# Optimization experiments

Measured on AMD Instinct MI355X. Metric: run time of the kernel, lower is better.

The kernel has to match this reference:

```python
import jax, jax.numpy as jnp
import numpy as np

# Module hyperparameters (from init_kwargs)
KH, KW = 3, 3
STRIDE_H = STRIDE_W = 1
PAD_H = PAD_W = 1
DIL_H = DIL_W = 1
DEFORM_GROUPS = 1
IN_CH, OUT_CH = 64, 64


def setup_inputs() -> dict:
    key = jax.random.key(0)
    k1, k2, k3, k4 = jax.random.split(key, 4)
    B, C, H, W = 4, IN_CH, 128, 128
    K = KH * KW
    x = jax.random.normal(k1, (B, C, H, W), dtype=jnp.float32)
    offset = jax.random.normal(k2, (B, DEFORM_GROUPS * 2 * K, H, W), dtype=jnp.float32)
    mask = jax.random.uniform(k3, (B, DEFORM_GROUPS * K, H, W), dtype=jnp.float32)
    stdv = 1.0 / np.sqrt(C * KH * KW)
    weight = jax.random.uniform(k4, (OUT_CH, C, KH, KW), dtype=jnp.float32,
                                minval=-stdv, maxval=stdv)
    bias = jnp.zeros((OUT_CH,), dtype=jnp.float32)
    return {"x": x, "offset": offset, "mask": mask, "weight": weight, "bias": bias}


def _bilinear_gather(img, ys, xs):
    """img: [N,Cg,H,W]; ys,xs: [N,K,Ho,Wo] absolute pixel coords.
    Returns [N,K,Ho,Wo,Cg]; zero padding outside, matches torch grid_sample
    (align_corners=False, padding_mode='zeros')."""
    N, Cg, H, W = img.shape
    y0f = jnp.floor(ys)
    x0f = jnp.floor(xs)
    wy = (ys - y0f)[..., None]
    wx = (xs - x0f)[..., None]
    y0 = y0f.astype(jnp.int32)
    x0 = x0f.astype(jnp.int32)
    b = jnp.arange(N)[:, None, None, None]

    def g(yi, xi):
        valid = (yi >= 0) & (yi < H) & (xi >= 0) & (xi < W)
        v = img[b, :, jnp.clip(yi, 0, H - 1), jnp.clip(xi, 0, W - 1)]  # [N,K,Ho,Wo,Cg]
        return jnp.where(valid[..., None], v, jnp.zeros((), img.dtype))

    v00 = g(y0, x0)
    v01 = g(y0, x0 + 1)
    v10 = g(y0 + 1, x0)
    v11 = g(y0 + 1, x0 + 1)
    return (v00 * (1 - wy) * (1 - wx) + v01 * (1 - wy) * wx
            + v10 * wy * (1 - wx) + v11 * wy * wx)


def _mdcn(x, offset, mask, weight, bias):
    B, C, H, W = x.shape
    O = weight.shape[0]
    K = KH * KW
    G = DEFORM_GROUPS
    Cg = C // G
    Ho = (H + 2 * PAD_H - (DIL_H * (KH - 1) + 1)) // STRIDE_H + 1
    Wo = (W + 2 * PAD_W - (DIL_W * (KW - 1) + 1)) // STRIDE_W + 1

    base_y = jnp.arange(Ho, dtype=x.dtype) * STRIDE_H - PAD_H          # [Ho]
    base_x = jnp.arange(Wo, dtype=x.dtype) * STRIDE_W - PAD_W          # [Wo]
    ky = (jnp.arange(K) // KW).astype(x.dtype) * DIL_H                 # [K]
    kx = (jnp.arange(K) % KW).astype(x.dtype) * DIL_W                  # [K]

    off = offset.reshape(B, G, K, 2, Ho, Wo)
    sy = (base_y[None, None, None, :, None] + ky[None, None, :, None, None]
          + off[:, :, :, 0])                                           # [B,G,K,Ho,Wo]
    sx = (base_x[None, None, None, None, :] + kx[None, None, :, None, None]
          + off[:, :, :, 1])

    img = x.reshape(B * G, Cg, H, W)
    sampled = _bilinear_gather(img, sy.reshape(B * G, K, Ho, Wo),
                               sx.reshape(B * G, K, Ho, Wo))            # [B*G,K,Ho,Wo,Cg]
    sampled = sampled * mask.reshape(B * G, K, Ho, Wo)[..., None]
    sampled = sampled.reshape(B, G, K, Ho, Wo, Cg)

    w = weight.reshape(O, G, Cg, K)
    out = jnp.einsum('bgkhwc,ogck->bohw', sampled, w)
    return out + bias[None, :, None, None]


def reference(x, offset, mask, weight, bias):
    return _mdcn(x, offset, mask, weight, bias)
```

## Files before the change

### kernel.cpp

```cpp
#include <hip/hip_runtime.h>
#include <hip/hip_bf16.h>
#include <math.h>

constexpr int B = 4, C = 64, H = 128, W = 128, K = 9, O = 64;
constexpr int HXW = H * W;

typedef _Float16 half8 __attribute__((ext_vector_type(8)));
typedef float f32x4 __attribute__((ext_vector_type(4)));

__global__ void wt_kernel(const float* __restrict__ weight, float* __restrict__ wt) {
    int idx = blockIdx.x * 256 + threadIdx.x;
    if (idx >= K * C * O) return;
    int o = idx & 63;
    int c = (idx >> 6) & 63;
    int k = idx >> 12;
    wt[idx] = weight[(o * C + c) * K + k];
}

__global__ __launch_bounds__(256) void mdcn_nchw(
        const float* __restrict__ x, const float* __restrict__ offset,
        const float* __restrict__ mask, const float* __restrict__ wt,
        const float* __restrict__ bias, float* __restrict__ out) {
    int pid = blockIdx.x * 256 + threadIdx.x;
    int b = pid >> 14;
    int hw = pid & (HXW - 1);
    int h = hw >> 7;
    int w = hw & 127;
    float acc[O];
#pragma unroll
    for (int o = 0; o < O; ++o) acc[o] = bias[o];
#pragma unroll 1
    for (int k = 0; k < K; ++k) {
        float offy = offset[((size_t)(b * 2 * K + 2 * k)) * HXW + hw];
        float offx = offset[((size_t)(b * 2 * K + 2 * k + 1)) * HXW + hw];
        float m    = mask[((size_t)(b * K + k)) * HXW + hw];
        float sy = (float)(h - 1 + k / 3) + offy;
        float sx = (float)(w - 1 + k % 3) + offx;
        float y0f = floorf(sy), x0f = floorf(sx);
        float wy = sy - y0f, wx = sx - x0f;
        int y0 = (int)y0f, x0 = (int)x0f;
        int y1 = y0 + 1, x1 = x0 + 1;
        bool vy0 = (y0 >= 0) & (y0 < H), vy1 = (y1 >= 0) & (y1 < H);
        bool vx0 = (x0 >= 0) & (x0 < W), vx1 = (x1 >= 0) & (x1 < W);
        float w00 = (vy0 & vx0) ? (1.0f - wy) * (1.0f - wx) * m : 0.0f;
        float w01 = (vy0 & vx1) ? (1.0f - wy) * wx * m : 0.0f;
        float w10 = (vy1 & vx0) ? wy * (1.0f - wx) * m : 0.0f;
        float w11 = (vy1 & vx1) ? wy * wx * m : 0.0f;
        int y0c = min(max(y0, 0), H - 1), y1c = min(max(y1, 0), H - 1);
        int x0c = min(max(x0, 0), W - 1), x1c = min(max(x1, 0), W - 1);
        const float* p00 = x + (size_t)b * C * HXW + y0c * W + x0c;
        const float* p01 = x + (size_t)b * C * HXW + y0c * W + x1c;
        const float* p10 = x + (size_t)b * C * HXW + y1c * W + x0c;
        const float* p11 = x + (size_t)b * C * HXW + y1c * W + x1c;
        const float* wk = wt + k * C * O;
#pragma unroll 1
        for (int c0 = 0; c0 < C; c0 += 4) {
            float v[4];
#pragma unroll
            for (int j = 0; j < 4; ++j) {
                size_t cs = (size_t)(c0 + j) * HXW;
                v[j] = w00 * p00[cs] + w01 * p01[cs] + w10 * p10[cs] + w11 * p11[cs];
            }
            const float* wr = wk + c0 * O;
#pragma unroll
            for (int j = 0; j < 4; ++j)
#pragma unroll
                for (int o = 0; o < O; ++o) acc[o] = fmaf(wr[j * O + o], v[j], acc[o]);
        }
    }
#pragma unroll
    for (int o = 0; o < O; ++o) out[((size_t)(b * O + o)) * HXW + hw] = acc[o];
}

constexpr int XT_BLOCKS = B * HXW / 128;
__global__ __launch_bounds__(256) void prep_kernel(
        const float* __restrict__ x, const float* __restrict__ weight,
        _Float16* __restrict__ xht, _Float16* __restrict__ wth) {
    int bid = blockIdx.x;
    if (bid < XT_BLOCKS) {
        __shared__ float lds[128 * 65];
        int t = threadIdx.x;
        int P = bid * 128;
        int b = P >> 14;
        int hw0 = P & (HXW - 1);
        int px = t & 127;
        int hf = t >> 7;
        const float* src = x + (size_t)b * C * HXW + hw0 + px;
#pragma unroll
        for (int cc = 0; cc < 32; ++cc) {
            int ch = hf * 32 + cc;
            lds[px * 65 + ch] = src[(size_t)ch * HXW];
        }
        __syncthreads();
        _Float16* dst = xht + ((size_t)b * HXW + hw0 + px) * 64 + hf * 32;
        const float* row = lds + px * 65 + hf * 32;
#pragma unroll
        for (int j = 0; j < 4; ++j) {
            half8 pk;
#pragma unroll
            for (int e = 0; e < 8; ++e) pk[e] = (_Float16)row[j * 8 + e];
            *(half8*)(dst + j * 8) = pk;
        }
    } else {
        int idx = (bid - XT_BLOCKS) * 256 + threadIdx.x;
        if (idx < K * O * C) {
            int e = idx & 7;
            int lane = (idx >> 3) & 63;
            int s = (idx >> 9) & 7;
            int k = idx >> 12;
            int ml = lane & 15, kg = lane >> 4;
            int nf = s & 3, ks = s >> 2;
            int o = nf * 16 + ml;
            int c = ks * 32 + kg * 8 + e;
            wth[idx] = (_Float16)weight[(o * C + c) * K + k];
        }
    }
}

__global__ __launch_bounds__(1024, 1) void mdcn_f16(
        const _Float16* __restrict__ xht,
        const float* __restrict__ offset,
        const float* __restrict__ mask,
        const _Float16* __restrict__ wth,
        const float* __restrict__ bias,
        float* __restrict__ out) {
    __shared__ _Float16 Wlds[K * 8 * 64 * 8];
    __shared__ _Float16 Alds[16][16 * 64];

    int bid = blockIdx.x;
    int slab = bid & 7;
    int within = bid >> 3;
    int tid = threadIdx.x;
    int lane = tid & 63;
    int wid = tid >> 6;
    int ml = lane & 15, kg = lane >> 4;
    int p8 = lane >> 3, ch8 = lane & 7;
    int b = slab >> 1;
    int hwblk = (slab & 1) * 8192 + within * 256;
    int h = (hwblk >> 7) + (wid >> 3);
    int wbase = (wid & 7) * 16;
    int hwwave = h * 128 + wbase;
    _Float16* Aw = &Alds[wid][0];

#pragma unroll
    for (int j = 0; j < 5; ++j) {
        int idx = tid + j * 1024;
        if (idx < K * 8 * 64) *(half8*)(Wlds + idx * 8) = *(const half8*)(wth + idx * 8);
    }
    __syncthreads();

    f32x4 acc[4];
#pragma unroll
    for (int nf = 0; nf < 4; ++nf) {
        float bv = bias[nf * 16 + ml];
        acc[nf] = (f32x4){bv, bv, bv, bv};
    }

    const _Float16* xb = xht + (size_t)b * HXW * 64;
    const float* offb = offset + (size_t)b * 2 * K * HXW;
    const float* mskb = mask + (size_t)b * K * HXW;

    float oy[2], ox[2], mm[2];
#pragma unroll
    for (int g = 0; g < 2; ++g) {
        int hw = hwwave + g * 8 + p8;
        oy[g] = offb[hw];
        ox[g] = offb[(size_t)HXW + hw];
        mm[g] = mskb[hw];
    }

#pragma unroll 1
    for (int k = 0; k < K; ++k) {
        int ky = k / 3 - 1, kx = k % 3 - 1;

        float w00[2], w01[2], w10[2], w11[2];
        int r00[2], r01[2], r10[2], r11[2];
#pragma unroll
        for (int g = 0; g < 2; ++g) {
            int pl = g * 8 + p8;
            int w = wbase + pl;
            float sy = (float)(h + ky) + oy[g];
            float sx = (float)(w + kx) + ox[g];
            float y0f = floorf(sy), x0f = floorf(sx);
            float wy = sy - y0f, wx = sx - x0f;
            int y0 = (int)y0f, x0 = (int)x0f;
            int y1 = y0 + 1, x1 = x0 + 1;
            bool vy0 = (y0 >= 0) & (y0 < H), vy1 = (y1 >= 0) & (y1 < H);
            bool vx0 = (x0 >= 0) & (x0 < W), vx1 = (x1 >= 0) & (x1 < W);
            float m = mm[g];
            w00[g] = (vy0 & vx0) ? (1.0f - wy) * (1.0f - wx) * m : 0.0f;
            w01[g] = (vy0 & vx1) ? (1.0f - wy) * wx * m : 0.0f;
            w10[g] = (vy1 & vx0) ? wy * (1.0f - wx) * m : 0.0f;
            w11[g] = (vy1 & vx1) ? wy * wx * m : 0.0f;
            int y0c = min(max(y0, 0), H - 1), y1c = min(max(y1, 0), H - 1);
            int x0c = min(max(x0, 0), W - 1), x1c = min(max(x1, 0), W - 1);
            r00[g] = y0c * W + x0c;
            r01[g] = y0c * W + x1c;
            r10[g] = y1c * W + x0c;
            r11[g] = y1c * W + x1c;
        }

        half8 c00[2], c01[2], c10[2], c11[2];
#pragma unroll
        for (int g = 0; g < 2; ++g) {
            c00[g] = *(const half8*)(xb + r00[g] * 64 + ch8 * 8);
            c01[g] = *(const half8*)(xb + r01[g] * 64 + ch8 * 8);
            c10[g] = *(const half8*)(xb + r10[g] * 64 + ch8 * 8);
            c11[g] = *(const half8*)(xb + r11[g] * 64 + ch8 * 8);
        }

        float oy2[2], ox2[2], mm2[2];
        if (k + 1 < K) {
#pragma unroll
            for (int g = 0; g < 2; ++g) {
                int hw = hwwave + g * 8 + p8;
                oy2[g] = offb[(size_t)(2 * k + 2) * HXW + hw];
                ox2[g] = offb[(size_t)(2 * k + 3) * HXW + hw];
                mm2[g] = mskb[(size_t)(k + 1) * HXW + hw];
            }
        }
        __builtin_amdgcn_sched_barrier(0);

#pragma unroll
        for (int g = 0; g < 2; ++g) {
            int pl = g * 8 + p8;
            _Float16 h00 = (_Float16)w00[g], h01 = (_Float16)w01[g];
            _Float16 h10 = (_Float16)w10[g], h11 = (_Float16)w11[g];
            half8 pk = c00[g] * h00 + c01[g] * h01 + c10[g] * h10 + c11[g] * h11;
            *(half8*)(Aw + pl * 64 + ((ch8 ^ (pl & 7)) * 8)) = pk;
        }

#pragma unroll
        for (int ks = 0; ks < 2; ++ks) {
            half8 af = *(const half8*)(Aw + ml * 64 + (((ks * 4 + kg) ^ (ml & 7)) * 8));
#pragma unroll
            for (int nf = 0; nf < 4; ++nf) {
                half8 bfr = *(const half8*)(Wlds + ((k * 8 + ks * 4 + nf) * 64 + lane) * 8);
                acc[nf] = __builtin_amdgcn_mfma_f32_16x16x32_f16(af, bfr, acc[nf], 0, 0, 0);
            }
        }

        if (k + 1 < K) {
#pragma unroll
            for (int g = 0; g < 2; ++g) { oy[g] = oy2[g]; ox[g] = ox2[g]; mm[g] = mm2[g]; }
        }
    }

    int hwb = hwwave + kg * 4;
#pragma unroll
    for (int nf = 0; nf < 4; ++nf) {
        size_t ob = ((size_t)(b * O + nf * 16 + ml)) * HXW + hwb;
        *(float4*)(out + ob) = __builtin_bit_cast(float4, acc[nf]);
    }
}

extern "C" void kernel_launch(void* const* d_in, const int* in_sizes, int n_in,
                              void* d_out, int out_size, void* d_ws, size_t ws_size,
                              hipStream_t stream) {
    const float* x      = (const float*)d_in[0];
    const float* offset = (const float*)d_in[1];
    const float* mask   = (const float*)d_in[2];
    const float* weight = (const float*)d_in[3];
    const float* bias   = (const float*)d_in[4];
    float* out = (float*)d_out;

    _Float16* wth = (_Float16*)d_ws;
    _Float16* xht = (_Float16*)((char*)d_ws + 73728);
    size_t need = 73728 + (size_t)B * HXW * 64 * sizeof(_Float16);

    if (ws_size >= need) {
        int wth_blocks = (K * O * C + 255) / 256;
        prep_kernel<<<XT_BLOCKS + wth_blocks, 256, 0, stream>>>(x, weight, xht, wth);
        mdcn_f16<<<256, 1024, 0, stream>>>(xht, offset, mask, wth, bias, out);
    } else {
        float* wt = (float*)d_ws;
        wt_kernel<<<(K * C * O + 255) / 256, 256, 0, stream>>>(weight, wt);
        mdcn_nchw<<<(B * HXW) / 256, 256, 0, stream>>>(x, offset, mask, wt, bias, out);
    }
}
```

Before: 36.42 us.

## Double-buffer bilinear gathers to prefetch next tap while computing current

Restructures the per-tap loop into a software pipeline. Sampling metadata and the four-corner gathers for tap k+1 are issued before tap k is blended and fed to MFMA, and offsets for k+2 are prefetched. The loop is fully unrolled so the double-buffer indices resolve at compile time. The aim is to hide global gather latency behind compute, at the cost of more registers and possibly lower occupancy.

```diff
diff --git a/kernel.cpp b/kernel.cpp
--- a/kernel.cpp
+++ b/kernel.cpp
@@ -161,24 +161,24 @@
     const float* mskb = mask + (size_t)b * K * HXW;
 
     float oy[2], ox[2], mm[2];
-#pragma unroll
-    for (int g = 0; g < 2; ++g) {
-        int hw = hwwave + g * 8 + p8;
-        oy[g] = offb[hw];
-        ox[g] = offb[(size_t)HXW + hw];
-        mm[g] = mskb[hw];
-    }
-
-#pragma unroll 1
-    for (int k = 0; k < K; ++k) {
+    float w00[2][2], w01[2][2], w10[2][2], w11[2][2];
+    int rr00[2][2], rr01[2][2], rr10[2][2], rr11[2][2];
+    half8 c00[2][2], c01[2][2], c10[2][2], c11[2][2];
+
+    auto load_off = [&](int k) {
+#pragma unroll
+        for (int g = 0; g < 2; ++g) {
+            int hw = hwwave + g * 8 + p8;
+            oy[g] = offb[(size_t)(2 * k) * HXW + hw];
+            ox[g] = offb[(size_t)(2 * k + 1) * HXW + hw];
+            mm[g] = mskb[(size_t)k * HXW + hw];
+        }
+    };
+    auto make_meta = [&](int k, int bu) {
         int ky = k / 3 - 1, kx = k % 3 - 1;
-
-        float w00[2], w01[2], w10[2], w11[2];
-        int r00[2], r01[2], r10[2], r11[2];
-#pragma unroll
-        for (int g = 0; g < 2; ++g) {
-            int pl = g * 8 + p8;
-            int w = wbase + pl;
+#pragma unroll
+        for (int g = 0; g < 2; ++g) {
+            int w = wbase + g * 8 + p8;
             float sy = (float)(h + ky) + oy[g];
             float sx = (float)(w + kx) + ox[g];
             float y0f = floorf(sy), x0f = floorf(sx);
@@ -188,45 +188,51 @@
             bool vy0 = (y0 >= 0) & (y0 < H), vy1 = (y1 >= 0) & (y1 < H);
             bool vx0 = (x0 >= 0) & (x0 < W), vx1 = (x1 >= 0) & (x1 < W);
             float m = mm[g];
-            w00[g] = (vy0 & vx0) ? (1.0f - wy) * (1.0f - wx) * m : 0.0f;
-            w01[g] = (vy0 & vx1) ? (1.0f - wy) * wx * m : 0.0f;
-            w10[g] = (vy1 & vx0) ? wy * (1.0f - wx) * m : 0.0f;
-            w11[g] = (vy1 & vx1) ? wy * wx * m : 0.0f;
+            w00[bu][g] = (vy0 & vx0) ? (1.0f - wy) * (1.0f - wx) * m : 0.0f;
+            w01[bu][g] = (vy0 & vx1) ? (1.0f - wy) * wx * m : 0.0f;
+            w10[bu][g] = (vy1 & vx0) ? wy * (1.0f - wx) * m : 0.0f;
+            w11[bu][g] = (vy1 & vx1) ? wy * wx * m : 0.0f;
             int y0c = min(max(y0, 0), H - 1), y1c = min(max(y1, 0), H - 1);
             int x0c = min(max(x0, 0), W - 1), x1c = min(max(x1, 0), W - 1);
-            r00[g] = y0c * W + x0c;
-            r01[g] = y0c * W + x1c;
-            r10[g] = y1c * W + x0c;
-            r11[g] = y1c * W + x1c;
-        }
-
-        half8 c00[2], c01[2], c10[2], c11[2];
-#pragma unroll
-        for (int g = 0; g < 2; ++g) {
-            c00[g] = *(const half8*)(xb + r00[g] * 64 + ch8 * 8);
-            c01[g] = *(const half8*)(xb + r01[g] * 64 + ch8 * 8);
-            c10[g] = *(const half8*)(xb + r10[g] * 64 + ch8 * 8);
-            c11[g] = *(const half8*)(xb + r11[g] * 64 + ch8 * 8);
-        }
-
-        float oy2[2], ox2[2], mm2[2];
+            rr00[bu][g] = y0c * W + x0c;
+            rr01[bu][g] = y0c * W + x1c;
+            rr10[bu][g] = y1c * W + x0c;
+            rr11[bu][g] = y1c * W + x1c;
+        }
+    };
+    auto issue_gather = [&](int bu) {
+#pragma unroll
+        for (int g = 0; g < 2; ++g) {
+            c00[bu][g] = *(const half8*)(xb + rr00[bu][g] * 64 + ch8 * 8);
+            c01[bu][g] = *(const half8*)(xb + rr01[bu][g] * 64 + ch8 * 8);
+            c10[bu][g] = *(const half8*)(xb + rr10[bu][g] * 64 + ch8 * 8);
+            c11[bu][g] = *(const half8*)(xb + rr11[bu][g] * 64 + ch8 * 8);
+        }
+    };
+
+    load_off(0);
+    make_meta(0, 0);
+    issue_gather(0);
+    load_off(1);
+
+#pragma unroll
+    for (int k = 0; k < K; ++k) {
+        const int cur = k & 1, nxt = cur ^ 1;
+
         if (k + 1 < K) {
-#pragma unroll
-            for (int g = 0; g < 2; ++g) {
-                int hw = hwwave + g * 8 + p8;
-                oy2[g] = offb[(size_t)(2 * k + 2) * HXW + hw];
-                ox2[g] = offb[(size_t)(2 * k + 3) * HXW + hw];
-                mm2[g] = mskb[(size_t)(k + 1) * HXW + hw];
-            }
-        }
+            make_meta(k + 1, nxt);
+            issue_gather(nxt);
+        }
+        if (k + 2 < K) load_off(k + 2);
         __builtin_amdgcn_sched_barrier(0);
 
 #pragma unroll
         for (int g = 0; g < 2; ++g) {
             int pl = g * 8 + p8;
-            _Float16 h00 = (_Float16)w00[g], h01 = (_Float16)w01[g];
-            _Float16 h10 = (_Float16)w10[g], h11 = (_Float16)w11[g];
-            half8 pk = c00[g] * h00 + c01[g] * h01 + c10[g] * h10 + c11[g] * h11;
+            _Float16 h00 = (_Float16)w00[cur][g], h01 = (_Float16)w01[cur][g];
+            _Float16 h10 = (_Float16)w10[cur][g], h11 = (_Float16)w11[cur][g];
+            half8 pk = c00[cur][g] * h00 + c01[cur][g] * h01 +
+                       c10[cur][g] * h10 + c11[cur][g] * h11;
             *(half8*)(Aw + pl * 64 + ((ch8 ^ (pl & 7)) * 8)) = pk;
         }
 
@@ -238,11 +244,6 @@
                 half8 bfr = *(const half8*)(Wlds + ((k * 8 + ks * 4 + nf) * 64 + lane) * 8);
                 acc[nf] = __builtin_amdgcn_mfma_f32_16x16x32_f16(af, bfr, acc[nf], 0, 0, 0);
             }
-        }
-
-        if (k + 1 < K) {
-#pragma unroll
-            for (int g = 0; g < 2; ++g) { oy[g] = oy2[g]; ox[g] = ox2[g]; mm[g] = mm2[g]; }
         }
     }
 
```

After: 44.23 us. +21.4%, slower.

## Split kernel taps across two wave halves and reduce partial sums in LDS

Applied to the files above, without the earlier changes.

The main kernel now launches 1024 blocks of 512 threads instead of 256 blocks of 1024. Each block covers 64 pixels, and the nine kernel taps are split between two groups of four waves (5 taps and 4 taps). The second group writes its partial accumulators to padded LDS, and the first group adds them in before storing the output. The per-block LDS weight staging and its barrier are removed, so weight fragments are read straight from global memory (through the cache) inside the MFMA loop. The intent is more blocks and waves for better occupancy and latency hiding on the 256-CU device, at the cost of repeated global weight loads, an extra LDS reduction, and unbalanced work between the two halves.

```diff
diff --git a/kernel.cpp b/kernel.cpp
--- a/kernel.cpp
+++ b/kernel.cpp
@@ -117,15 +117,15 @@
     }
 }
 
-__global__ __launch_bounds__(1024, 1) void mdcn_f16(
+__global__ __launch_bounds__(512, 8) void mdcn_f16(
         const _Float16* __restrict__ xht,
         const float* __restrict__ offset,
         const float* __restrict__ mask,
         const _Float16* __restrict__ wth,
         const float* __restrict__ bias,
         float* __restrict__ out) {
-    __shared__ _Float16 Wlds[K * 8 * 64 * 8];
-    __shared__ _Float16 Alds[16][16 * 64];
+    __shared__ _Float16 Alds[8][16 * 64];
+    __shared__ float Rlds[64 * 65];
 
     int bid = blockIdx.x;
     int slab = bid & 7;
@@ -133,26 +133,21 @@
     int tid = threadIdx.x;
     int lane = tid & 63;
     int wid = tid >> 6;
+    int pxgrp = wid & 3;
+    int half = wid >> 2;
     int ml = lane & 15, kg = lane >> 4;
     int p8 = lane >> 3, ch8 = lane & 7;
     int b = slab >> 1;
-    int hwblk = (slab & 1) * 8192 + within * 256;
-    int h = (hwblk >> 7) + (wid >> 3);
-    int wbase = (wid & 7) * 16;
+    int hwbase = (slab & 1) * 8192 + within * 64;
+    int h = hwbase >> 7;
+    int wbase = (hwbase & 127) + pxgrp * 16;
     int hwwave = h * 128 + wbase;
     _Float16* Aw = &Alds[wid][0];
 
-#pragma unroll
-    for (int j = 0; j < 5; ++j) {
-        int idx = tid + j * 1024;
-        if (idx < K * 8 * 64) *(half8*)(Wlds + idx * 8) = *(const half8*)(wth + idx * 8);
-    }
-    __syncthreads();
-
     f32x4 acc[4];
 #pragma unroll
     for (int nf = 0; nf < 4; ++nf) {
-        float bv = bias[nf * 16 + ml];
+        float bv = (half == 0) ? bias[nf * 16 + ml] : 0.0f;
         acc[nf] = (f32x4){bv, bv, bv, bv};
     }
 
@@ -160,25 +155,28 @@
     const float* offb = offset + (size_t)b * 2 * K * HXW;
     const float* mskb = mask + (size_t)b * K * HXW;
 
+    int k0 = half * 5;
+    int nt = 5 - half;
+
     float oy[2], ox[2], mm[2];
 #pragma unroll
     for (int g = 0; g < 2; ++g) {
         int hw = hwwave + g * 8 + p8;
-        oy[g] = offb[hw];
-        ox[g] = offb[(size_t)HXW + hw];
-        mm[g] = mskb[hw];
+        oy[g] = offb[(size_t)(2 * k0) * HXW + hw];
+        ox[g] = offb[(size_t)(2 * k0 + 1) * HXW + hw];
+        mm[g] = mskb[(size_t)k0 * HXW + hw];
     }
 
 #pragma unroll 1
-    for (int k = 0; k < K; ++k) {
+    for (int kk = 0; kk < nt; ++kk) {
+        int k = k0 + kk;
         int ky = k / 3 - 1, kx = k % 3 - 1;
 
         float w00[2], w01[2], w10[2], w11[2];
         int r00[2], r01[2], r10[2], r11[2];
 #pragma unroll
         for (int g = 0; g < 2; ++g) {
-            int pl = g * 8 + p8;
-            int w = wbase + pl;
+            int w = wbase + g * 8 + p8;
             float sy = (float)(h + ky) + oy[g];
             float sx = (float)(w + kx) + ox[g];
             float y0f = floorf(sy), x0f = floorf(sx);
@@ -210,7 +208,7 @@
         }
 
         float oy2[2], ox2[2], mm2[2];
-        if (k + 1 < K) {
+        if (kk + 1 < nt) {
 #pragma unroll
             for (int g = 0; g < 2; ++g) {
                 int hw = hwwave + g * 8 + p8;
@@ -235,22 +233,36 @@
             half8 af = *(const half8*)(Aw + ml * 64 + (((ks * 4 + kg) ^ (ml & 7)) * 8));
 #pragma unroll
             for (int nf = 0; nf < 4; ++nf) {
-                half8 bfr = *(const half8*)(Wlds + ((k * 8 + ks * 4 + nf) * 64 + lane) * 8);
+                half8 bfr = *(const half8*)(wth + ((size_t)((k * 8 + ks * 4 + nf) * 64 + lane)) * 8);
                 acc[nf] = __builtin_amdgcn_mfma_f32_16x16x32_f16(af, bfr, acc[nf], 0, 0, 0);
             }
         }
 
-        if (k + 1 < K) {
+        if (kk + 1 < nt) {
 #pragma unroll
             for (int g = 0; g < 2; ++g) { oy[g] = oy2[g]; ox[g] = ox2[g]; mm[g] = mm2[g]; }
         }
     }
 
-    int hwb = hwwave + kg * 4;
-#pragma unroll
-    for (int nf = 0; nf < 4; ++nf) {
-        size_t ob = ((size_t)(b * O + nf * 16 + ml)) * HXW + hwb;
-        *(float4*)(out + ob) = __builtin_bit_cast(float4, acc[nf]);
+    if (half == 1) {
+#pragma unroll
+        for (int nf = 0; nf < 4; ++nf)
+#pragma unroll
+            for (int r = 0; r < 4; ++r)
+                Rlds[(pxgrp * 16 + kg * 4 + r) * 65 + nf * 16 + ml] = acc[nf][r];
+    }
+    __syncthreads();
+    if (half == 0) {
+        int hwb = hwwave + kg * 4;
+#pragma unroll
+        for (int nf = 0; nf < 4; ++nf) {
+            f32x4 v = acc[nf];
+#pragma unroll
+            for (int r = 0; r < 4; ++r)
+                v[r] += Rlds[(pxgrp * 16 + kg * 4 + r) * 65 + nf * 16 + ml];
+            size_t ob = ((size_t)(b * O + nf * 16 + ml)) * HXW + hwb;
+            *(float4*)(out + ob) = __builtin_bit_cast(float4, v);
+        }
     }
 }
 
@@ -271,7 +283,7 @@
     if (ws_size >= need) {
         int wth_blocks = (K * O * C + 255) / 256;
         prep_kernel<<<XT_BLOCKS + wth_blocks, 256, 0, stream>>>(x, weight, xht, wth);
-        mdcn_f16<<<256, 1024, 0, stream>>>(xht, offset, mask, wth, bias, out);
+        mdcn_f16<<<1024, 512, 0, stream>>>(xht, offset, mask, wth, bias, out);
     } else {
         float* wt = (float*)d_ws;
         wt_kernel<<<(K * C * O + 255) / 256, 256, 0, stream>>>(weight, wt);
```

Result: slower. 96.06 us (+163.7%).
